# Performance work log

Measured on AMD Instinct MI355X. Metric: run time of the kernel, lower is better.

## Reference

```python
import jax, jax.numpy as jnp
import numpy as np
import math

N_H = 16

def _rope(x):
    # x: [b, h, n, d_k]; standard RoPE with half-split rotation
    n, d_k = x.shape[2], x.shape[3]
    inv_freq = 1.0 / (10000.0 ** (jnp.arange(0, d_k, 2, dtype=jnp.float32) / d_k))  # [d_k/2]
    freqs = jnp.arange(n, dtype=jnp.float32)[:, None] * inv_freq[None, :]            # [n, d_k/2]
    cos = jnp.concatenate([jnp.cos(freqs), jnp.cos(freqs)], axis=-1)[None, None]     # [1,1,n,d_k]
    sin = jnp.concatenate([jnp.sin(freqs), jnp.sin(freqs)], axis=-1)[None, None]
    x1, x2 = jnp.split(x, 2, axis=-1)
    rot = jnp.concatenate([-x2, x1], axis=-1)
    return x * cos + rot * sin


def setup_inputs() -> dict:
    key = jax.random.key(0)
    k1, k2, k3, k4 = jax.random.split(key, 4)
    b, n, d_m = 2, 1024, 2048
    x = jax.random.normal(k1, (b, n, d_m), dtype=jnp.float32)
    # causal mask (1 = keep, 0 = masked)
    m = jnp.tril(jnp.ones((n, n), dtype=jnp.int32))[None, None]  # [1,1,n,n]
    s = 1.0 / math.sqrt(d_m)
    Wqkv = jax.random.normal(k2, (d_m, 3 * d_m), dtype=jnp.float32) * s
    Wout = jax.random.normal(k3, (d_m, d_m), dtype=jnp.float32) * s
    bout = jax.random.normal(k4, (d_m,), dtype=jnp.float32) * 0.01
    return {"x": x, "m": m, "Wqkv": Wqkv, "Wout": Wout, "bout": bout}


def reference(x, m, Wqkv, Wout, bout):
    b, n, d = x.shape
    d_k = d // N_H
    qkv = (x @ Wqkv).reshape(b, n, 3, N_H, d_k)
    qkv = jnp.transpose(qkv, (2, 0, 3, 1, 4))  # [3, b, h, n, d_k]
    q, k, v = qkv[0], qkv[1], qkv[2]
    q, k = _rope(q), _rope(k)
    s = jnp.einsum('bhqd,bhkd->bhqk', q, k) / math.sqrt(d_k)
    s = jnp.where(m == 0, -jnp.inf, s)
    a = jax.nn.softmax(s, axis=-1)  # dropout is identity in eval / drop=0
    r = jnp.einsum('bhqk,bhkd->bhqd', a, v)
    r = jnp.transpose(r, (0, 2, 1, 3)).reshape(b, n, d)
    return r @ Wout + bout
```

## Files before the change

### kernel.cpp

```cpp
#include <hip/hip_runtime.h>
#include <math.h>

typedef unsigned short u16;
typedef unsigned int u32;
typedef __attribute__((ext_vector_type(8))) short short8;
typedef __attribute__((ext_vector_type(4))) float f32x4;

#define DEVI __device__ __forceinline__

DEVI u16 f2bf(float x) {
    union { float f; u32 u; } un; un.f = x;
    u32 u = un.u;
    return (u16)((u + 0x7fffu + ((u >> 16) & 1u)) >> 16);
}
DEVI float bf2f(u16 v) {
    union { u32 u; float f; } un; un.u = ((u32)v) << 16;
    return un.f;
}
DEVI f32x4 mfma_bf16(short8 a, short8 b, f32x4 c) {
    return __builtin_amdgcn_mfma_f32_16x16x32_bf16(a, b, c, 0, 0, 0);
}
DEVI void gload_lds16(const void* g, void* l) {
    __builtin_amdgcn_global_load_lds((const __attribute__((address_space(1))) u32*)g,
                                     (__attribute__((address_space(3))) u32*)l,
                                     16, 0, 0);
}

__global__ void k_prep(const float* __restrict__ x, const float* __restrict__ Wqkv,
                       const float* __restrict__ Wout, u16* __restrict__ x_bf,
                       u16* __restrict__ WqkvT, u16* __restrict__ WoutT) {
    __shared__ u16 tile[64][68];
    const int bid = blockIdx.x;
    if (bid < 4096) {
        long idx = ((long)bid * 256 + threadIdx.x) * 4;
        float4 v = *(const float4*)(x + idx);
        ushort4 o;
        o.x = f2bf(v.x); o.y = f2bf(v.y); o.z = f2bf(v.z); o.w = f2bf(v.w);
        *(ushort4*)(x_bf + idx) = o;
        return;
    }
    const float* in;
    u16* out;
    int R, C, bx, by;
    if (bid < 7168) {
        int lb = bid - 4096;
        in = Wqkv; out = WqkvT; R = 2048; C = 6144;
        bx = lb % 96; by = lb / 96;
    } else {
        int lb = bid - 7168;
        in = Wout; out = WoutT; R = 2048; C = 2048;
        bx = lb & 31; by = lb >> 5;
    }
    const int tx = threadIdx.x & 15, ty = threadIdx.x >> 4;
    const long r0 = (long)by * 64, c0 = (long)bx * 64;
#pragma unroll
    for (int p = 0; p < 4; ++p) {
        int r = ty + p * 16;
        float4 v = *(const float4*)(in + (r0 + r) * C + c0 + tx * 4);
        ushort4 o;
        o.x = f2bf(v.x); o.y = f2bf(v.y); o.z = f2bf(v.z); o.w = f2bf(v.w);
        *(ushort4*)&tile[r][tx * 4] = o;
    }
    __syncthreads();
#pragma unroll
    for (int p = 0; p < 4; ++p) {
        int rr = ty + p * 16;
        ushort4 o;
        o.x = tile[tx * 4 + 0][rr];
        o.y = tile[tx * 4 + 1][rr];
        o.z = tile[tx * 4 + 2][rr];
        o.w = tile[tx * 4 + 3][rr];
        *(ushort4*)(out + (c0 + rr) * R + r0 + tx * 4) = o;
    }
}

template <int EPI>
__global__ __launch_bounds__(256, 2) void k_gemm(const u16* __restrict__ A,
                                                 const u16* __restrict__ BT, int K,
                                                 u16* __restrict__ qb, u16* __restrict__ kb,
                                                 u16* __restrict__ vtb, float* __restrict__ out,
                                                 const float* __restrict__ bias) {
    __shared__ union SM {
        struct { u16 As[128 * 64]; u16 Bs[128 * 64]; } s;
        u16 T[128 * 132];
    } sm;
    const int tid = threadIdx.x;
    const int lane = tid & 63, wave = tid >> 6;
    const int lm = lane & 15, quad = lane >> 4;
    const int wm = wave >> 1, wn = wave & 1;
    const int bm = blockIdx.x, bn = blockIdx.y;

    f32x4 acc[4][4] = {};

    const int srow = lane >> 3;
    const int scb = (lane & 7) ^ srow;
    const long arow0 = (long)bm * 128;
    const long brow0 = (long)bn * 128;

    for (int k0 = 0; k0 < K; k0 += 64) {
        __syncthreads();
#pragma unroll
        for (int it = 0; it < 4; ++it) {
            int ch = wave * 4 + it;
            long r = ch * 8 + srow;
            gload_lds16(A + (arow0 + r) * K + k0 + scb * 8, (char*)sm.s.As + ch * 1024);
            gload_lds16(BT + (brow0 + r) * K + k0 + scb * 8, (char*)sm.s.Bs + ch * 1024);
        }
        __syncthreads();
#pragma unroll
        for (int ko = 0; ko < 2; ++ko) {
            short8 af[4], bf[4];
#pragma unroll
            for (int i = 0; i < 4; ++i) {
                int row = wm * 64 + i * 16 + lm;
                int pc = (ko * 4 + quad) ^ (lm & 7);
                af[i] = *(const short8*)&sm.s.As[row * 64 + pc * 8];
            }
#pragma unroll
            for (int j = 0; j < 4; ++j) {
                int row = wn * 64 + j * 16 + lm;
                int pc = (ko * 4 + quad) ^ (lm & 7);
                bf[j] = *(const short8*)&sm.s.Bs[row * 64 + pc * 8];
            }
#pragma unroll
            for (int i = 0; i < 4; ++i)
#pragma unroll
                for (int j = 0; j < 4; ++j)
                    acc[i][j] = mfma_bf16(af[i], bf[j], acc[i][j]);
        }
    }

    if constexpr (EPI == 0) {
        __syncthreads();
#pragma unroll
        for (int i = 0; i < 4; ++i)
#pragma unroll
            for (int j = 0; j < 4; ++j) {
                const int col = wn * 64 + j * 16 + lm;
#pragma unroll
                for (int r = 0; r < 4; ++r) {
                    const int row = wm * 64 + i * 16 + quad * 4 + r;
                    sm.T[row * 132 + col] = f2bf(acc[i][j][r]);
                }
            }
        __syncthreads();
        const int which = bn >> 4, h = bn & 15, b = bm >> 3;
        const int p0 = (bm & 7) * 128;
        if (which < 2) {
            u16* dst = which ? kb : qb;
            const long hb = ((long)(b * 16 + h)) * 1024;
            const int i0 = (tid * 4) & 63;
            const int pb = tid >> 4;
            float inv[4];
#pragma unroll
            for (int e = 0; e < 4; ++e)
                inv[e] = exp2f(-(float)(i0 + e) * 0.20762050593045952f);
#pragma unroll
            for (int c = 0; c < 8; ++c) {
                const int pos_l = c * 16 + pb;
                ushort4 cur = *(const ushort4*)&sm.T[pos_l * 132 + i0];
                ushort4 par = *(const ushort4*)&sm.T[pos_l * 132 + i0 + 64];
                const float pg = (float)(p0 + pos_l);
                ushort4 o1, o2;
                const u16* cp = (const u16*)&cur;
                const u16* pp = (const u16*)&par;
                u16* o1p = (u16*)&o1;
                u16* o2p = (u16*)&o2;
#pragma unroll
                for (int e = 0; e < 4; ++e) {
                    float th = pg * inv[e];
                    float sv = __sinf(th), cv = __cosf(th);
                    float x1 = bf2f(cp[e]), x2 = bf2f(pp[e]);
                    o1p[e] = f2bf(x1 * cv - x2 * sv);
                    o2p[e] = f2bf(x2 * cv + x1 * sv);
                }
                const long rowb = (hb + p0 + pos_l) * 128;
                *(ushort4*)(dst + rowb + i0) = o1;
                *(ushort4*)(dst + rowb + i0 + 64) = o2;
            }
        } else {
            const long vrow = ((long)(b * 16 + h)) * 128;
#pragma unroll
            for (int c = 0; c < 8; ++c) {
                const int lin = c * 2048 + tid * 8;
                const int dk = lin >> 7;
                const int ps = lin & 127;
                ushort4 o1, o2;
                u16* o1p = (u16*)&o1;
                u16* o2p = (u16*)&o2;
#pragma unroll
                for (int e = 0; e < 4; ++e) {
                    o1p[e] = sm.T[(ps + e) * 132 + dk];
                    o2p[e] = sm.T[(ps + 4 + e) * 132 + dk];
                }
                u16* dst = vtb + (vrow + dk) * 1024 + p0 + ps;
                *(ushort4*)dst = o1;
                *(ushort4*)(dst + 4) = o2;
            }
        }
    } else {
        float bv[4];
#pragma unroll
        for (int j = 0; j < 4; ++j) bv[j] = bias[bn * 128 + wn * 64 + j * 16 + lm];
#pragma unroll
        for (int i = 0; i < 4; ++i) {
#pragma unroll
            for (int r = 0; r < 4; ++r) {
                const int row = bm * 128 + wm * 64 + i * 16 + quad * 4 + r;
#pragma unroll
                for (int j = 0; j < 4; ++j) {
                    const int col = bn * 128 + wn * 64 + j * 16 + lm;
                    out[(long)row * 2048 + col] = acc[i][j][r] + bv[j];
                }
            }
        }
    }
}

__global__ __launch_bounds__(256, 2) void k_flash(const u16* __restrict__ Q,
                                                  const u16* __restrict__ Kb,
                                                  const u16* __restrict__ VT,
                                                  u16* __restrict__ R) {
    __shared__ u16 Ks[64 * 128];
    __shared__ u16 Vs[128 * 64];
    __shared__ u16 Ps[64 * 72];
    const int tid = threadIdx.x;
    const int lane = tid & 63, wave = tid >> 6;
    const int lm = lane & 15, quad = lane >> 4;
    const int id = blockIdx.x;
    const int g = id >> 8, rem = id & 255;
    const int bh = rem >> 3, s = rem & 7;
    const int qt = g ? (15 - s) : s;
    const long qkbase = (long)bh * 1024 * 128;
    const long vtbase = (long)bh * 128 * 1024;
    const int q0 = qt * 64;

    short8 qf[4];
    {
        const u16* qrow = Q + qkbase + (long)(q0 + wave * 16 + lm) * 128 + quad * 8;
#pragma unroll
        for (int kc = 0; kc < 4; ++kc) qf[kc] = *(const short8*)(qrow + kc * 32);
    }

    f32x4 o_acc[8] = {};
    float m_i = -INFINITY, l_i = 0.f;
    const float cl2e = 0.08838834764831845f * 1.4426950408889634f;

    const int kr = lane >> 4;
    const int vr = lane >> 3;
    const int vcb = (lane & 7) ^ vr;

    for (int kt = 0; kt <= qt; ++kt) {
        __syncthreads();
        {
#pragma unroll
            for (int it = 0; it < 4; ++it) {
                int ch = wave * 4 + it;
                int krow = ch * 4 + kr;
                int kchunk = (lane & 15) ^ (krow & 15);
                gload_lds16(Kb + qkbase + (long)(kt * 64 + krow) * 128 + kchunk * 8,
                            (char*)Ks + ch * 1024);
                int vrow = ch * 8 + vr;
                gload_lds16(VT + vtbase + (long)vrow * 1024 + kt * 64 + vcb * 8,
                            (char*)Vs + ch * 1024);
            }
        }
        __syncthreads();

        f32x4 s_acc[4] = {};
#pragma unroll
        for (int kc = 0; kc < 4; ++kc) {
#pragma unroll
            for (int mi = 0; mi < 4; ++mi) {
                int row = mi * 16 + lm;
                int pc = (kc * 4 + quad) ^ lm;
                short8 ak = *(const short8*)&Ks[row * 128 + pc * 8];
                s_acc[mi] = mfma_bf16(ak, qf[kc], s_acc[mi]);
            }
        }
        const int qg = q0 + wave * 16 + lm;
        float t[4][4];
        float cmax = -INFINITY;
#pragma unroll
        for (int mi = 0; mi < 4; ++mi)
#pragma unroll
            for (int r = 0; r < 4; ++r) {
                int kg = kt * 64 + mi * 16 + quad * 4 + r;
                float val = (kg <= qg) ? s_acc[mi][r] * cl2e : -INFINITY;
                t[mi][r] = val;
                cmax = fmaxf(cmax, val);
            }
        cmax = fmaxf(cmax, __shfl_xor(cmax, 16));
        cmax = fmaxf(cmax, __shfl_xor(cmax, 32));
        float m_new = fmaxf(m_i, cmax);
        float alpha = exp2f(m_i - m_new);
        float csum = 0.f;
#pragma unroll
        for (int mi = 0; mi < 4; ++mi)
#pragma unroll
            for (int r = 0; r < 4; ++r) {
                float p = exp2f(t[mi][r] - m_new);
                t[mi][r] = p;
                csum += p;
            }
        csum += __shfl_xor(csum, 16);
        csum += __shfl_xor(csum, 32);
        l_i = l_i * alpha + csum;
        m_i = m_new;
#pragma unroll
        for (int mi = 0; mi < 4; ++mi) {
            ushort4 pk;
            pk.x = f2bf(t[mi][0]); pk.y = f2bf(t[mi][1]);
            pk.z = f2bf(t[mi][2]); pk.w = f2bf(t[mi][3]);
            *(ushort4*)&Ps[(wave * 16 + lm) * 72 + mi * 16 + quad * 4] = pk;
        }
        float aq[4];
#pragma unroll
        for (int r = 0; r < 4; ++r) aq[r] = __shfl(alpha, quad * 4 + r, 64);
#pragma unroll
        for (int nt = 0; nt < 8; ++nt)
#pragma unroll
            for (int r = 0; r < 4; ++r) o_acc[nt][r] *= aq[r];
#pragma unroll
        for (int kc = 0; kc < 2; ++kc) {
            short8 ap = *(const short8*)&Ps[(wave * 16 + lm) * 72 + kc * 32 + quad * 8];
#pragma unroll
            for (int nt = 0; nt < 8; ++nt) {
                int row = nt * 16 + lm;
                int pc = (kc * 4 + quad) ^ (lm & 7);
                short8 bv = *(const short8*)&Vs[row * 64 + pc * 8];
                o_acc[nt] = mfma_bf16(ap, bv, o_acc[nt]);
            }
        }
    }
    float lq[4];
#pragma unroll
    for (int r = 0; r < 4; ++r) lq[r] = __shfl(l_i, quad * 4 + r, 64);
    const int b = bh >> 4, h = bh & 15;
#pragma unroll
    for (int nt = 0; nt < 8; ++nt)
#pragma unroll
        for (int r = 0; r < 4; ++r) {
            const int pos = q0 + wave * 16 + quad * 4 + r;
            const int col = h * 128 + nt * 16 + lm;
            R[((long)b * 1024 + pos) * 2048 + col] = f2bf(o_acc[nt][r] / lq[r]);
        }
}

extern "C" void kernel_launch(void* const* d_in, const int* in_sizes, int n_in,
                              void* d_out, int out_size, void* d_ws, size_t ws_size,
                              hipStream_t stream) {
    const float* x    = (const float*)d_in[0];
    const float* Wqkv = (const float*)d_in[2];
    const float* Wout = (const float*)d_in[3];
    const float* bout = (const float*)d_in[4];
    float* out = (float*)d_out;

    char* ws = (char*)d_ws;
    u16* x_bf  = (u16*)(ws);
    u16* rbuf  = x_bf;
    u16* WqkvT = (u16*)(ws + (8L << 20));
    u16* WoutT = (u16*)(ws + (32L << 20));
    u16* qbuf  = (u16*)(ws + (40L << 20));
    u16* kbuf  = (u16*)(ws + (48L << 20));
    u16* vtbuf = (u16*)(ws + (56L << 20));

    k_prep<<<8192, 256, 0, stream>>>(x, Wqkv, Wout, x_bf, WqkvT, WoutT);
    k_gemm<0><<<dim3(16, 48), 256, 0, stream>>>(x_bf, WqkvT, 2048, qbuf, kbuf, vtbuf,
                                                nullptr, nullptr);
    k_flash<<<512, 256, 0, stream>>>(qbuf, kbuf, vtbuf, rbuf);
    k_gemm<1><<<dim3(16, 16), 256, 0, stream>>>(rbuf, WoutT, 2048, nullptr, nullptr, nullptr,
                                                out, bout);
}
```

Baseline: 248.5 us.

## Overlap Wout transpose with flash attention, retile output GEMM, skip off-diagonal masking

Moves the Wout fp32-to-bf16 transpose out of the prep kernel and into extra blocks of the flash-attention launch, so it fills idle CUs during the causal attention tail. The output projection GEMM now uses 64x128 tiles, which doubles its block count to 512 for better CU coverage. Only the diagonal key tile applies causal masking, and launch bounds rise to 3 blocks per CU. The costs are lower per-block reuse in the output GEMM and the flash kernel sharing the GPU with transpose blocks.

Measured after the change: 245.6 us. About the same (-1.2%).

```diff
diff --git a/kernel.cpp b/kernel.cpp
--- a/kernel.cpp
+++ b/kernel.cpp
@@ -26,9 +26,33 @@
                                      16, 0, 0);
 }
 
+DEVI void transpose_tile_64(const float* __restrict__ in, u16* __restrict__ out,
+                            int R, int C, int bx, int by, int tidx, u16 (*tile)[68]) {
+    const int tx = tidx & 15, ty = tidx >> 4;
+    const long r0 = (long)by * 64, c0 = (long)bx * 64;
+#pragma unroll
+    for (int p = 0; p < 4; ++p) {
+        int r = ty + p * 16;
+        float4 v = *(const float4*)(in + (r0 + r) * C + c0 + tx * 4);
+        ushort4 o;
+        o.x = f2bf(v.x); o.y = f2bf(v.y); o.z = f2bf(v.z); o.w = f2bf(v.w);
+        *(ushort4*)&tile[r][tx * 4] = o;
+    }
+    __syncthreads();
+#pragma unroll
+    for (int p = 0; p < 4; ++p) {
+        int rr = ty + p * 16;
+        ushort4 o;
+        o.x = tile[tx * 4 + 0][rr];
+        o.y = tile[tx * 4 + 1][rr];
+        o.z = tile[tx * 4 + 2][rr];
+        o.w = tile[tx * 4 + 3][rr];
+        *(ushort4*)(out + (c0 + rr) * R + r0 + tx * 4) = o;
+    }
+}
+
 __global__ void k_prep(const float* __restrict__ x, const float* __restrict__ Wqkv,
-                       const float* __restrict__ Wout, u16* __restrict__ x_bf,
-                       u16* __restrict__ WqkvT, u16* __restrict__ WoutT) {
+                       u16* __restrict__ x_bf, u16* __restrict__ WqkvT) {
     __shared__ u16 tile[64][68];
     const int bid = blockIdx.x;
     if (bid < 4096) {
@@ -39,48 +63,16 @@
         *(ushort4*)(x_bf + idx) = o;
         return;
     }
-    const float* in;
-    u16* out;
-    int R, C, bx, by;
-    if (bid < 7168) {
-        int lb = bid - 4096;
-        in = Wqkv; out = WqkvT; R = 2048; C = 6144;
-        bx = lb % 96; by = lb / 96;
-    } else {
-        int lb = bid - 7168;
-        in = Wout; out = WoutT; R = 2048; C = 2048;
-        bx = lb & 31; by = lb >> 5;
-    }
-    const int tx = threadIdx.x & 15, ty = threadIdx.x >> 4;
-    const long r0 = (long)by * 64, c0 = (long)bx * 64;
-#pragma unroll
-    for (int p = 0; p < 4; ++p) {
-        int r = ty + p * 16;
-        float4 v = *(const float4*)(in + (r0 + r) * C + c0 + tx * 4);
-        ushort4 o;
-        o.x = f2bf(v.x); o.y = f2bf(v.y); o.z = f2bf(v.z); o.w = f2bf(v.w);
-        *(ushort4*)&tile[r][tx * 4] = o;
-    }
-    __syncthreads();
-#pragma unroll
-    for (int p = 0; p < 4; ++p) {
-        int rr = ty + p * 16;
-        ushort4 o;
-        o.x = tile[tx * 4 + 0][rr];
-        o.y = tile[tx * 4 + 1][rr];
-        o.z = tile[tx * 4 + 2][rr];
-        o.w = tile[tx * 4 + 3][rr];
-        *(ushort4*)(out + (c0 + rr) * R + r0 + tx * 4) = o;
-    }
-}
-
-template <int EPI>
-__global__ __launch_bounds__(256, 2) void k_gemm(const u16* __restrict__ A,
-                                                 const u16* __restrict__ BT, int K,
-                                                 u16* __restrict__ qb, u16* __restrict__ kb,
-                                                 u16* __restrict__ vtb, float* __restrict__ out,
-                                                 const float* __restrict__ bias) {
-    __shared__ union SM {
+    int lb = bid - 4096;
+    transpose_tile_64(Wqkv, WqkvT, 2048, 6144, lb % 96, lb / 96, threadIdx.x, tile);
+}
+
+__global__ __launch_bounds__(256, 3) void k_gemm_qkv(const u16* __restrict__ A,
+                                                     const u16* __restrict__ BT,
+                                                     u16* __restrict__ qb, u16* __restrict__ kb,
+                                                     u16* __restrict__ vtb) {
+    constexpr int K = 2048;
+    __shared__ __align__(16) union SM {
         struct { u16 As[128 * 64]; u16 Bs[128 * 64]; } s;
         u16 T[128 * 132];
     } sm;
@@ -130,104 +122,168 @@
         }
     }
 
-    if constexpr (EPI == 0) {
-        __syncthreads();
-#pragma unroll
-        for (int i = 0; i < 4; ++i)
+    __syncthreads();
+#pragma unroll
+    for (int i = 0; i < 4; ++i)
+#pragma unroll
+        for (int j = 0; j < 4; ++j) {
+            const int col = wn * 64 + j * 16 + lm;
+#pragma unroll
+            for (int r = 0; r < 4; ++r) {
+                const int row = wm * 64 + i * 16 + quad * 4 + r;
+                sm.T[row * 132 + col] = f2bf(acc[i][j][r]);
+            }
+        }
+    __syncthreads();
+    const int which = bn >> 4, h = bn & 15, b = bm >> 3;
+    const int p0 = (bm & 7) * 128;
+    if (which < 2) {
+        u16* dst = which ? kb : qb;
+        const long hb = ((long)(b * 16 + h)) * 1024;
+        const int i0 = (tid * 4) & 63;
+        const int pb = tid >> 4;
+        float inv[4];
+#pragma unroll
+        for (int e = 0; e < 4; ++e)
+            inv[e] = exp2f(-(float)(i0 + e) * 0.20762050593045952f);
+#pragma unroll
+        for (int c = 0; c < 8; ++c) {
+            const int pos_l = c * 16 + pb;
+            ushort4 cur = *(const ushort4*)&sm.T[pos_l * 132 + i0];
+            ushort4 par = *(const ushort4*)&sm.T[pos_l * 132 + i0 + 64];
+            const float pg = (float)(p0 + pos_l);
+            ushort4 o1, o2;
+            const u16* cp = (const u16*)&cur;
+            const u16* pp = (const u16*)&par;
+            u16* o1p = (u16*)&o1;
+            u16* o2p = (u16*)&o2;
+#pragma unroll
+            for (int e = 0; e < 4; ++e) {
+                float th = pg * inv[e];
+                float sv = __sinf(th), cv = __cosf(th);
+                float x1 = bf2f(cp[e]), x2 = bf2f(pp[e]);
+                o1p[e] = f2bf(x1 * cv - x2 * sv);
+                o2p[e] = f2bf(x2 * cv + x1 * sv);
+            }
+            const long rowb = (hb + p0 + pos_l) * 128;
+            *(ushort4*)(dst + rowb + i0) = o1;
+            *(ushort4*)(dst + rowb + i0 + 64) = o2;
+        }
+    } else {
+        const long vrow = ((long)(b * 16 + h)) * 128;
+#pragma unroll
+        for (int c = 0; c < 8; ++c) {
+            const int lin = c * 2048 + tid * 8;
+            const int dk = lin >> 7;
+            const int ps = lin & 127;
+            ushort4 o1, o2;
+            u16* o1p = (u16*)&o1;
+            u16* o2p = (u16*)&o2;
+#pragma unroll
+            for (int e = 0; e < 4; ++e) {
+                o1p[e] = sm.T[(ps + e) * 132 + dk];
+                o2p[e] = sm.T[(ps + 4 + e) * 132 + dk];
+            }
+            u16* dst = vtb + (vrow + dk) * 1024 + p0 + ps;
+            *(ushort4*)dst = o1;
+            *(ushort4*)(dst + 4) = o2;
+        }
+    }
+}
+
+__global__ __launch_bounds__(256, 3) void k_gemm_out(const u16* __restrict__ A,
+                                                     const u16* __restrict__ BT,
+                                                     float* __restrict__ out,
+                                                     const float* __restrict__ bias) {
+    constexpr int K = 2048;
+    __shared__ __align__(16) struct { u16 As[64 * 64]; u16 Bs[128 * 64]; } sm;
+    const int tid = threadIdx.x;
+    const int lane = tid & 63, wave = tid >> 6;
+    const int lm = lane & 15, quad = lane >> 4;
+    const int wm = wave >> 1, wn = wave & 1;
+    const int bm = blockIdx.x, bn = blockIdx.y;
+
+    f32x4 acc[2][4] = {};
+
+    const int srow = lane >> 3;
+    const int scb = (lane & 7) ^ srow;
+    const long arow0 = (long)bm * 64;
+    const long brow0 = (long)bn * 128;
+
+    for (int k0 = 0; k0 < K; k0 += 64) {
+        __syncthreads();
+#pragma unroll
+        for (int it = 0; it < 2; ++it) {
+            int ch = wave * 2 + it;
+            long r = ch * 8 + srow;
+            gload_lds16(A + (arow0 + r) * K + k0 + scb * 8, (char*)sm.As + ch * 1024);
+        }
+#pragma unroll
+        for (int it = 0; it < 4; ++it) {
+            int ch = wave * 4 + it;
+            long r = ch * 8 + srow;
+            gload_lds16(BT + (brow0 + r) * K + k0 + scb * 8, (char*)sm.Bs + ch * 1024);
+        }
+        __syncthreads();
+#pragma unroll
+        for (int ko = 0; ko < 2; ++ko) {
+            short8 af[2], bf[4];
+#pragma unroll
+            for (int i = 0; i < 2; ++i) {
+                int row = wm * 32 + i * 16 + lm;
+                int pc = (ko * 4 + quad) ^ (lm & 7);
+                af[i] = *(const short8*)&sm.As[row * 64 + pc * 8];
+            }
 #pragma unroll
             for (int j = 0; j < 4; ++j) {
-                const int col = wn * 64 + j * 16 + lm;
-#pragma unroll
-                for (int r = 0; r < 4; ++r) {
-                    const int row = wm * 64 + i * 16 + quad * 4 + r;
-                    sm.T[row * 132 + col] = f2bf(acc[i][j][r]);
-                }
-            }
-        __syncthreads();
-        const int which = bn >> 4, h = bn & 15, b = bm >> 3;
-        const int p0 = (bm & 7) * 128;
-        if (which < 2) {
-            u16* dst = which ? kb : qb;
-            const long hb = ((long)(b * 16 + h)) * 1024;
-            const int i0 = (tid * 4) & 63;
-            const int pb = tid >> 4;
-            float inv[4];
-#pragma unroll
-            for (int e = 0; e < 4; ++e)
-                inv[e] = exp2f(-(float)(i0 + e) * 0.20762050593045952f);
-#pragma unroll
-            for (int c = 0; c < 8; ++c) {
-                const int pos_l = c * 16 + pb;
-                ushort4 cur = *(const ushort4*)&sm.T[pos_l * 132 + i0];
-                ushort4 par = *(const ushort4*)&sm.T[pos_l * 132 + i0 + 64];
-                const float pg = (float)(p0 + pos_l);
-                ushort4 o1, o2;
-                const u16* cp = (const u16*)&cur;
-                const u16* pp = (const u16*)&par;
-                u16* o1p = (u16*)&o1;
-                u16* o2p = (u16*)&o2;
-#pragma unroll
-                for (int e = 0; e < 4; ++e) {
-                    float th = pg * inv[e];
-                    float sv = __sinf(th), cv = __cosf(th);
-                    float x1 = bf2f(cp[e]), x2 = bf2f(pp[e]);
-                    o1p[e] = f2bf(x1 * cv - x2 * sv);
-                    o2p[e] = f2bf(x2 * cv + x1 * sv);
-                }
-                const long rowb = (hb + p0 + pos_l) * 128;
-                *(ushort4*)(dst + rowb + i0) = o1;
-                *(ushort4*)(dst + rowb + i0 + 64) = o2;
-            }
-        } else {
-            const long vrow = ((long)(b * 16 + h)) * 128;
-#pragma unroll
-            for (int c = 0; c < 8; ++c) {
-                const int lin = c * 2048 + tid * 8;
-                const int dk = lin >> 7;
-                const int ps = lin & 127;
-                ushort4 o1, o2;
-                u16* o1p = (u16*)&o1;
-                u16* o2p = (u16*)&o2;
-#pragma unroll
-                for (int e = 0; e < 4; ++e) {
-                    o1p[e] = sm.T[(ps + e) * 132 + dk];
-                    o2p[e] = sm.T[(ps + 4 + e) * 132 + dk];
-                }
-                u16* dst = vtb + (vrow + dk) * 1024 + p0 + ps;
-                *(ushort4*)dst = o1;
-                *(ushort4*)(dst + 4) = o2;
-            }
-        }
-    } else {
-        float bv[4];
-#pragma unroll
-        for (int j = 0; j < 4; ++j) bv[j] = bias[bn * 128 + wn * 64 + j * 16 + lm];
-#pragma unroll
-        for (int i = 0; i < 4; ++i) {
-#pragma unroll
-            for (int r = 0; r < 4; ++r) {
-                const int row = bm * 128 + wm * 64 + i * 16 + quad * 4 + r;
-#pragma unroll
-                for (int j = 0; j < 4; ++j) {
-                    const int col = bn * 128 + wn * 64 + j * 16 + lm;
-                    out[(long)row * 2048 + col] = acc[i][j][r] + bv[j];
-                }
-            }
-        }
-    }
-}
-
-__global__ __launch_bounds__(256, 2) void k_flash(const u16* __restrict__ Q,
+                int row = wn * 64 + j * 16 + lm;
+                int pc = (ko * 4 + quad) ^ (lm & 7);
+                bf[j] = *(const short8*)&sm.Bs[row * 64 + pc * 8];
+            }
+#pragma unroll
+            for (int i = 0; i < 2; ++i)
+#pragma unroll
+                for (int j = 0; j < 4; ++j)
+                    acc[i][j] = mfma_bf16(af[i], bf[j], acc[i][j]);
+        }
+    }
+
+    float bv[4];
+#pragma unroll
+    for (int j = 0; j < 4; ++j) bv[j] = bias[bn * 128 + wn * 64 + j * 16 + lm];
+#pragma unroll
+    for (int i = 0; i < 2; ++i) {
+#pragma unroll
+        for (int r = 0; r < 4; ++r) {
+            const int row = bm * 64 + wm * 32 + i * 16 + quad * 4 + r;
+#pragma unroll
+            for (int j = 0; j < 4; ++j) {
+                const int col = bn * 128 + wn * 64 + j * 16 + lm;
+                out[(long)row * 2048 + col] = acc[i][j][r] + bv[j];
+            }
+        }
+    }
+}
+
+__global__ __launch_bounds__(256, 3) void k_flash(const u16* __restrict__ Q,
                                                   const u16* __restrict__ Kb,
                                                   const u16* __restrict__ VT,
-                                                  u16* __restrict__ R) {
+                                                  u16* __restrict__ R,
+                                                  const float* __restrict__ Wout,
+                                                  u16* __restrict__ WoutT) {
     __shared__ u16 Ks[64 * 128];
     __shared__ u16 Vs[128 * 64];
     __shared__ u16 Ps[64 * 72];
     const int tid = threadIdx.x;
+    const int id = blockIdx.x;
+    if (id >= 512) {
+        const int lb = id - 512;
+        transpose_tile_64(Wout, WoutT, 2048, 2048, lb & 31, lb >> 5, tid,
+                          (u16(*)[68])Ks);
+        return;
+    }
     const int lane = tid & 63, wave = tid >> 6;
     const int lm = lane & 15, quad = lane >> 4;
-    const int id = blockIdx.x;
     const int g = id >> 8, rem = id & 255;
     const int bh = rem >> 3, s = rem & 7;
     const int qt = g ? (15 - s) : s;
@@ -278,18 +334,29 @@
                 s_acc[mi] = mfma_bf16(ak, qf[kc], s_acc[mi]);
             }
         }
-        const int qg = q0 + wave * 16 + lm;
         float t[4][4];
         float cmax = -INFINITY;
-#pragma unroll
-        for (int mi = 0; mi < 4; ++mi)
-#pragma unroll
-            for (int r = 0; r < 4; ++r) {
-                int kg = kt * 64 + mi * 16 + quad * 4 + r;
-                float val = (kg <= qg) ? s_acc[mi][r] * cl2e : -INFINITY;
-                t[mi][r] = val;
-                cmax = fmaxf(cmax, val);
-            }
+        if (kt == qt) {
+            const int qg = q0 + wave * 16 + lm;
+#pragma unroll
+            for (int mi = 0; mi < 4; ++mi)
+#pragma unroll
+                for (int r = 0; r < 4; ++r) {
+                    int kg = kt * 64 + mi * 16 + quad * 4 + r;
+                    float val = (kg <= qg) ? s_acc[mi][r] * cl2e : -INFINITY;
+                    t[mi][r] = val;
+                    cmax = fmaxf(cmax, val);
+                }
+        } else {
+#pragma unroll
+            for (int mi = 0; mi < 4; ++mi)
+#pragma unroll
+                for (int r = 0; r < 4; ++r) {
+                    float val = s_acc[mi][r] * cl2e;
+                    t[mi][r] = val;
+                    cmax = fmaxf(cmax, val);
+                }
+        }
         cmax = fmaxf(cmax, __shfl_xor(cmax, 16));
         cmax = fmaxf(cmax, __shfl_xor(cmax, 32));
         float m_new = fmaxf(m_i, cmax);
@@ -365,10 +432,8 @@
     u16* kbuf  = (u16*)(ws + (48L << 20));
     u16* vtbuf = (u16*)(ws + (56L << 20));
 
-    k_prep<<<8192, 256, 0, stream>>>(x, Wqkv, Wout, x_bf, WqkvT, WoutT);
-    k_gemm<0><<<dim3(16, 48), 256, 0, stream>>>(x_bf, WqkvT, 2048, qbuf, kbuf, vtbuf,
-                                                nullptr, nullptr);
-    k_flash<<<512, 256, 0, stream>>>(qbuf, kbuf, vtbuf, rbuf);
-    k_gemm<1><<<dim3(16, 16), 256, 0, stream>>>(rbuf, WoutT, 2048, nullptr, nullptr, nullptr,
-                                                out, bout);
-}
+    k_prep<<<7168, 256, 0, stream>>>(x, Wqkv, x_bf, WqkvT);
+    k_gemm_qkv<<<dim3(16, 48), 256, 0, stream>>>(x_bf, WqkvT, qbuf, kbuf, vtbuf);
+    k_flash<<<1536, 256, 0, stream>>>(qbuf, kbuf, vtbuf, rbuf, Wout, WoutT);
+    k_gemm_out<<<dim3(32, 16), 256, 0, stream>>>(rbuf, WoutT, out, bout);
+}
```
